# Kernel tuning notes

Hardware: AMD Instinct MI355X
Metric: run time of the kernel (lower is better)

## Reference

```python
import jax, jax.numpy as jnp
import numpy as np

EMB = 768
HEADS = 12
HEAD_DIM = EMB // HEADS
SEQ = 4096
BATCH = 1


def setup_inputs() -> dict:
    key = jax.random.key(0)
    ks = jax.random.split(key, 9)
    s = 1.0 / np.sqrt(EMB)
    return {
        "x": jax.random.normal(ks[0], (BATCH, SEQ, EMB), dtype=jnp.float32),
        "wq": jax.random.normal(ks[1], (EMB, EMB), dtype=jnp.float32) * s,
        "bq": jax.random.normal(ks[2], (EMB,), dtype=jnp.float32) * s,
        "wk": jax.random.normal(ks[3], (EMB, EMB), dtype=jnp.float32) * s,
        "bk": jax.random.normal(ks[4], (EMB,), dtype=jnp.float32) * s,
        "wv": jax.random.normal(ks[5], (EMB, EMB), dtype=jnp.float32) * s,
        "bv": jax.random.normal(ks[6], (EMB,), dtype=jnp.float32) * s,
        "wo": jax.random.normal(ks[7], (EMB, EMB), dtype=jnp.float32) * s,
        "bo": jax.random.normal(ks[8], (EMB,), dtype=jnp.float32) * s,
    }


def reference(x, wq, bq, wk, bk, wv, bv, wo, bo):
    b, n, _ = x.shape
    # projections: [b, n, emb] -> [b, heads, n, head_dim]
    def split_heads(t):
        return t.reshape(b, n, HEADS, HEAD_DIM).transpose(0, 2, 1, 3)
    q = split_heads(x @ wq + bq)
    k = split_heads(x @ wk + bk)
    v = split_heads(x @ wv + bv)
    # full N x N scores (naive attention, as in the original)
    scores = jnp.einsum("bhqd,bhkd->bhqk", q, k)
    causal = jnp.triu(jnp.ones((n, n), dtype=bool), k=1)
    scores = jnp.where(causal, -jnp.inf, scores)
    weights = jax.nn.softmax(scores / np.sqrt(HEAD_DIM), axis=-1)
    # dropout with rate 0.0 is identity (eval mode)
    ctx = jnp.einsum("bhqk,bhkd->bhqd", weights, v)
    ctx = ctx.transpose(0, 2, 1, 3).reshape(b, n, EMB)
    return ctx @ wo + bo
```

## Files before the change

### kernel.cpp

```cpp
#include <hip/hip_runtime.h>
#include <stdint.h>

#define SEQ 4096
#define EMB 768
#define HEADS 12
#define HD 64
#define NQT (SEQ / 64)

typedef __attribute__((ext_vector_type(8))) short short8;
typedef __attribute__((ext_vector_type(4))) short short4v;
typedef __attribute__((ext_vector_type(8))) __bf16 bf16x8;
typedef __attribute__((ext_vector_type(4))) __bf16 bf16x4;
typedef __attribute__((ext_vector_type(4))) float f32x4;

#define QSCALE 0.18033688011112043f

static __device__ __forceinline__ unsigned short f2bf(float f) {
    unsigned int u = __builtin_bit_cast(unsigned int, f);
    unsigned int r = 0x7fffu + ((u >> 16) & 1u);
    u += r;
    return (unsigned short)(u >> 16);
}

static __device__ __forceinline__ f32x4 mfma32(short8 a, short8 b, f32x4 c) {
    return __builtin_amdgcn_mfma_f32_16x16x32_bf16(
        __builtin_bit_cast(bf16x8, a), __builtin_bit_cast(bf16x8, b), c, 0, 0, 0);
}

static __device__ __forceinline__ f32x4 mfma16(short4v a, short4v b, f32x4 c) {
#if __has_builtin(__builtin_amdgcn_mfma_f32_16x16x16_bf16)
    return __builtin_amdgcn_mfma_f32_16x16x16_bf16(
        __builtin_bit_cast(bf16x4, a), __builtin_bit_cast(bf16x4, b), c, 0, 0, 0);
#else
    return __builtin_amdgcn_mfma_f32_16x16x16bf16_1k(a, b, c, 0, 0, 0);
#endif
}

static __device__ __forceinline__ short4v pack4bf(float a, float b, float c, float d) {
#if __has_builtin(__builtin_amdgcn_cvt_pk_bf16_f32)
    typedef __attribute__((ext_vector_type(2))) __bf16 bf16x2;
    bf16x2 lo = __builtin_amdgcn_cvt_pk_bf16_f32(a, b);
    bf16x2 hi = __builtin_amdgcn_cvt_pk_bf16_f32(c, d);
    uint2 u = {__builtin_bit_cast(unsigned int, lo), __builtin_bit_cast(unsigned int, hi)};
    return __builtin_bit_cast(short4v, u);
#else
    short4v p;
    p[0] = (short)f2bf(a); p[1] = (short)f2bf(b);
    p[2] = (short)f2bf(c); p[3] = (short)f2bf(d);
    return p;
#endif
}

static __device__ __forceinline__ void load_lds16(const void* g, void* l) {
    __builtin_amdgcn_global_load_lds(
        (const __attribute__((address_space(1))) unsigned int*)(uintptr_t)g,
        (__attribute__((address_space(3))) unsigned int*)(uintptr_t)l, 16, 0, 0);
}

__global__ __launch_bounds__(256) void convert_x(const float* __restrict__ x,
                                                 unsigned short* __restrict__ xb) {
    int i = blockIdx.x * 256 + threadIdx.x;
    float4 v = ((const float4*)x)[i];
    ushort4 o = {f2bf(v.x), f2bf(v.y), f2bf(v.z), f2bf(v.w)};
    ((ushort4*)xb)[i] = o;
}

__global__ __launch_bounds__(256) void convert_w(const float* __restrict__ wq,
                                                 const float* __restrict__ wk,
                                                 const float* __restrict__ wv,
                                                 const float* __restrict__ wo,
                                                 unsigned short* __restrict__ wqkvT,
                                                 unsigned short* __restrict__ woT) {
    __shared__ float Ls[64][65];
    const int z = blockIdx.z;
    const float* W = (z == 0) ? wq : (z == 1) ? wk : (z == 2) ? wv : wo;
    unsigned short* dst = (z < 3) ? (wqkvT + (size_t)z * EMB * EMB) : woT;
    const int k0 = blockIdx.x * 64, n0 = blockIdx.y * 64;
    const int r = threadIdx.x >> 2, c0 = (threadIdx.x & 3) * 16;
    for (int j = 0; j < 16; j += 4) {
        float4 v = *(const float4*)&W[(size_t)(k0 + r) * EMB + n0 + c0 + j];
        Ls[r][c0 + j] = v.x;
        Ls[r][c0 + j + 1] = v.y;
        Ls[r][c0 + j + 2] = v.z;
        Ls[r][c0 + j + 3] = v.w;
    }
    __syncthreads();
    unsigned short tmp[16];
    for (int j = 0; j < 16; j++) tmp[j] = f2bf(Ls[c0 + j][r]);
    *(uint4*)&dst[(size_t)(n0 + r) * EMB + k0 + c0] = *(uint4*)tmp;
    *(uint4*)&dst[(size_t)(n0 + r) * EMB + k0 + c0 + 8] = *(uint4*)(tmp + 8);
}

template <int MODE>
__global__ __launch_bounds__(256) void gemm128(const unsigned short* __restrict__ A,
                                               const unsigned short* __restrict__ Bt,
                                               const float* __restrict__ b0p,
                                               const float* __restrict__ b1p,
                                               const float* __restrict__ b2p,
                                               unsigned short* __restrict__ QKb,
                                               unsigned short* __restrict__ Vtb,
                                               float* __restrict__ outp) {
    __shared__ __align__(16) unsigned short As[128 * 32];
    __shared__ __align__(16) unsigned short Bs[128 * 32];
    const int tid = threadIdx.x;
    const int wave = tid >> 6, lane = tid & 63, quad = lane >> 4, l16 = lane & 15;
    const int m0 = blockIdx.x * 128, n0 = blockIdx.y * 128;
    const int wm = (wave >> 1) * 64, wn = (wave & 1) * 64;
    const int lrow = lane >> 2, lcol = (lane & 3) * 8;

    f32x4 acc[4][4] = {};

    for (int k0 = 0; k0 < EMB; k0 += 32) {
        __syncthreads();
        for (int t = 0; t < 2; t++) {
            int row = wave * 32 + t * 16 + lrow;
            load_lds16(&A[(size_t)(m0 + row) * EMB + k0 + lcol], &As[(wave * 2 + t) * 512]);
            load_lds16(&Bt[(size_t)(n0 + row) * EMB + k0 + lcol], &Bs[(wave * 2 + t) * 512]);
        }
        __syncthreads();
        short8 a[4], b[4];
        for (int i = 0; i < 4; i++) a[i] = *(const short8*)&As[(wm + i * 16 + l16) * 32 + quad * 8];
        for (int i = 0; i < 4; i++) b[i] = *(const short8*)&Bs[(wn + i * 16 + l16) * 32 + quad * 8];
        for (int i = 0; i < 4; i++)
            for (int j = 0; j < 4; j++) acc[i][j] = mfma32(a[i], b[j], acc[i][j]);
    }

    if (MODE == 1) {
        for (int i = 0; i < 4; i++)
            for (int j = 0; j < 4; j++) {
                int mbase = m0 + wm + i * 16 + quad * 4;
                int n = n0 + wn + j * 16 + l16;
                float bv = b0p[n];
                for (int r = 0; r < 4; r++) outp[(size_t)(mbase + r) * EMB + n] = acc[i][j][r] + bv;
            }
    } else {
        const int z = n0 / EMB;
        if (z < 2) {
            const float* bias = z ? b1p : b0p;
            const float sc = z ? 1.0f : QSCALE;
            for (int i = 0; i < 4; i++)
                for (int j = 0; j < 4; j++) {
                    int mbase = m0 + wm + i * 16 + quad * 4;
                    int n = n0 + wn + j * 16 + l16;
                    float bv = bias[n - z * EMB];
                    for (int r = 0; r < 4; r++)
                        QKb[(size_t)(mbase + r) * 1536 + n] = f2bf((acc[i][j][r] + bv) * sc);
                }
        } else {
            for (int i = 0; i < 4; i++)
                for (int j = 0; j < 4; j++) {
                    int mbase = m0 + wm + i * 16 + quad * 4;
                    int nn = n0 + wn + j * 16 + l16 - 2 * EMB;
                    int h = nn >> 6, d = nn & 63;
                    float bv = b2p[nn];
                    ushort4 pk;
                    pk.x = f2bf(acc[i][j][0] + bv);
                    pk.y = f2bf(acc[i][j][1] + bv);
                    pk.z = f2bf(acc[i][j][2] + bv);
                    pk.w = f2bf(acc[i][j][3] + bv);
                    *(ushort4*)&Vtb[(size_t)(h * HD + d) * SEQ + mbase] = pk;
                }
        }
    }
}

__global__ __launch_bounds__(256) void attn_kernel(const unsigned short* __restrict__ QKb,
                                                   const unsigned short* __restrict__ Vtb,
                                                   unsigned short* __restrict__ ctxb,
                                                   unsigned short* __restrict__ Op,
                                                   float* __restrict__ mArr,
                                                   float* __restrict__ lArr) {
    __shared__ __align__(16) unsigned short Qs[64 * 72];
    __shared__ __align__(16) unsigned short Ks[64 * 72];
    __shared__ __align__(16) unsigned short Vs[64 * 72];

    const int bid = blockIdx.x;
    int s, h, qt, kb, ke;
    if (bid < 768) {
        s = bid & 1;
        int idx = bid >> 1;
        qt = 63 - idx / 12;
        h = idx % 12;
        int h0 = (qt + 2) >> 1;
        kb = s ? h0 : 0;
        ke = s ? qt : h0 - 1;
    } else {
        s = -1;
        int idx = bid - 768;
        qt = 31 - idx / 12;
        h = idx % 12;
        kb = 0;
        ke = qt;
    }
    const int qbase = qt * 64;
    const int tid = threadIdx.x;
    const int wave = tid >> 6, lane = tid & 63, quad = lane >> 4, l16 = lane & 15;

    const unsigned short* Qg = QKb + (size_t)h * HD;
    const unsigned short* Kg = QKb + (size_t)(EMB + h * HD);
    const unsigned short* Vh = Vtb + (size_t)h * HD * SEQ;

    const int row = tid >> 2, cg = (tid & 3) * 16;
    *(uint4*)&Qs[row * 72 + cg] = *(const uint4*)&Qg[(size_t)(qbase + row) * 1536 + cg];
    *(uint4*)&Qs[row * 72 + cg + 8] = *(const uint4*)&Qg[(size_t)(qbase + row) * 1536 + cg + 8];
    __syncthreads();
    const short8 bQ0 = *(const short8*)&Qs[(wave * 16 + l16) * 72 + quad * 8];
    const short8 bQ1 = *(const short8*)&Qs[(wave * 16 + l16) * 72 + 32 + quad * 8];
    const int q = qbase + wave * 16 + l16;

    f32x4 O[4] = {};
    float m_i = -3.0e38f, l_i = 0.f;

    uint4 kr0, kr1, vr0, vr1;
    {
        const int kb64 = kb * 64;
        kr0 = *(const uint4*)&Kg[(size_t)(kb64 + row) * 1536 + cg];
        kr1 = *(const uint4*)&Kg[(size_t)(kb64 + row) * 1536 + cg + 8];
        vr0 = *(const uint4*)&Vh[(size_t)row * SEQ + kb64 + cg];
        vr1 = *(const uint4*)&Vh[(size_t)row * SEQ + kb64 + cg + 8];
    }

    for (int kt = kb; kt <= ke; kt++) {
        const int kbase = kt * 64;
        __syncthreads();
        *(uint4*)&Ks[row * 72 + cg] = kr0;
        *(uint4*)&Ks[row * 72 + cg + 8] = kr1;
        *(uint4*)&Vs[row * 72 + cg] = vr0;
        *(uint4*)&Vs[row * 72 + cg + 8] = vr1;
        if (kt < ke) {
            const int nb = kbase + 64;
            kr0 = *(const uint4*)&Kg[(size_t)(nb + row) * 1536 + cg];
            kr1 = *(const uint4*)&Kg[(size_t)(nb + row) * 1536 + cg + 8];
            vr0 = *(const uint4*)&Vh[(size_t)row * SEQ + nb + cg];
            vr1 = *(const uint4*)&Vh[(size_t)row * SEQ + nb + cg + 8];
        }
        __syncthreads();

        f32x4 st[4];
        for (int nt = 0; nt < 4; nt++) {
            short8 aK0 = *(const short8*)&Ks[(nt * 16 + l16) * 72 + quad * 8];
            short8 aK1 = *(const short8*)&Ks[(nt * 16 + l16) * 72 + 32 + quad * 8];
            f32x4 z = {};
            z = mfma32(aK0, bQ0, z);
            z = mfma32(aK1, bQ1, z);
            st[nt] = z;
        }
        if (kt == qt) {
            for (int nt = 0; nt < 4; nt++)
                for (int r = 0; r < 4; r++)
                    if (kbase + nt * 16 + quad * 4 + r > q) st[nt][r] = -INFINITY;
        }
        float mx = -3.0e38f;
        for (int nt = 0; nt < 4; nt++)
            for (int r = 0; r < 4; r++) mx = fmaxf(mx, st[nt][r]);
        mx = fmaxf(mx, __shfl_xor(mx, 16));
        mx = fmaxf(mx, __shfl_xor(mx, 32));
        const bool inc = mx > m_i;
        if (__ballot(inc)) {
            const float mn = inc ? mx : m_i;
            const float alpha = __builtin_amdgcn_exp2f(m_i - mn);
            m_i = mn;
            l_i *= alpha;
            for (int dt = 0; dt < 4; dt++)
                for (int r = 0; r < 4; r++) O[dt][r] *= alpha;
        }
        float rs = 0.f;
        short4v pk[4];
        for (int nt = 0; nt < 4; nt++) {
            float p0 = __builtin_amdgcn_exp2f(st[nt][0] - m_i);
            float p1 = __builtin_amdgcn_exp2f(st[nt][1] - m_i);
            float p2 = __builtin_amdgcn_exp2f(st[nt][2] - m_i);
            float p3 = __builtin_amdgcn_exp2f(st[nt][3] - m_i);
            rs += p0 + p1 + p2 + p3;
            pk[nt] = pack4bf(p0, p1, p2, p3);
        }
        rs += __shfl_xor(rs, 16);
        rs += __shfl_xor(rs, 32);
        l_i += rs;
        for (int dt = 0; dt < 4; dt++)
            for (int nt = 0; nt < 4; nt++) {
                short4v av = *(const short4v*)&Vs[(dt * 16 + l16) * 72 + nt * 16 + quad * 4];
                O[dt] = mfma16(av, pk[nt], O[dt]);
            }
    }

    const int ql = wave * 16 + l16;
    if (s < 0) {
        const float inv = 1.f / l_i;
        for (int dt = 0; dt < 4; dt++) {
            ushort4 o;
            o.x = f2bf(O[dt][0] * inv);
            o.y = f2bf(O[dt][1] * inv);
            o.z = f2bf(O[dt][2] * inv);
            o.w = f2bf(O[dt][3] * inv);
            *(ushort4*)&ctxb[(size_t)q * EMB + h * HD + dt * 16 + quad * 4] = o;
        }
    } else {
        const int pb = (s * HEADS + h) * 32 + (qt - 32);
        for (int dt = 0; dt < 4; dt++) {
            ushort4 o;
            o.x = f2bf(O[dt][0]);
            o.y = f2bf(O[dt][1]);
            o.z = f2bf(O[dt][2]);
            o.w = f2bf(O[dt][3]);
            *(ushort4*)&Op[(size_t)pb * 4096 + ql * 64 + dt * 16 + quad * 4] = o;
        }
        if (quad == 0) {
            mArr[pb * 64 + ql] = m_i;
            lArr[pb * 64 + ql] = l_i;
        }
    }
}

__global__ __launch_bounds__(256) void merge_kernel(const unsigned short* __restrict__ Op,
                                                    const float* __restrict__ mArr,
                                                    const float* __restrict__ lArr,
                                                    unsigned short* __restrict__ ctxb) {
    const int idx = blockIdx.x;
    const int qt = 32 + idx / HEADS;
    const int h = idx % HEADS;
    const int q = threadIdx.x >> 2, d0 = (threadIdx.x & 3) * 16;
    const int pb0 = h * 32 + (qt - 32);
    const int pb1 = (HEADS + h) * 32 + (qt - 32);
    const float m0 = mArr[pb0 * 64 + q], m1 = mArr[pb1 * 64 + q];
    const float l0 = lArr[pb0 * 64 + q], l1 = lArr[pb1 * 64 + q];
    const float M = fmaxf(m0, m1);
    float a0 = __builtin_amdgcn_exp2f(m0 - M);
    float a1 = __builtin_amdgcn_exp2f(m1 - M);
    const float inv = 1.f / (a0 * l0 + a1 * l1);
    a0 *= inv;
    a1 *= inv;
    for (int jj = 0; jj < 16; jj += 8) {
        uint4 u0 = *(const uint4*)&Op[(size_t)pb0 * 4096 + q * 64 + d0 + jj];
        uint4 u1 = *(const uint4*)&Op[(size_t)pb1 * 4096 + q * 64 + d0 + jj];
        const unsigned short* p0 = (const unsigned short*)&u0;
        const unsigned short* p1 = (const unsigned short*)&u1;
        unsigned short o[8];
        for (int t = 0; t < 8; t++) {
            float f0 = __builtin_bit_cast(float, (unsigned int)p0[t] << 16);
            float f1 = __builtin_bit_cast(float, (unsigned int)p1[t] << 16);
            o[t] = f2bf(a0 * f0 + a1 * f1);
        }
        *(uint4*)&ctxb[(size_t)(qt * 64 + q) * EMB + h * HD + d0 + jj] = *(uint4*)o;
    }
}

extern "C" void kernel_launch(void* const* d_in, const int* in_sizes, int n_in,
                              void* d_out, int out_size, void* d_ws, size_t ws_size,
                              hipStream_t stream) {
    const float* x = (const float*)d_in[0];
    const float* wq = (const float*)d_in[1];
    const float* bq = (const float*)d_in[2];
    const float* wk = (const float*)d_in[3];
    const float* bk = (const float*)d_in[4];
    const float* wv = (const float*)d_in[5];
    const float* bv = (const float*)d_in[6];
    const float* wo = (const float*)d_in[7];
    const float* bo = (const float*)d_in[8];

    unsigned short* ws = (unsigned short*)d_ws;
    unsigned short* xb = ws;
    unsigned short* wqkvT = xb + SEQ * EMB;
    unsigned short* woT = wqkvT + 3 * EMB * EMB;
    unsigned short* QKb = woT + EMB * EMB;
    unsigned short* Vtb = QKb + (size_t)SEQ * 1536;
    unsigned short* ctxb = Vtb + HEADS * SEQ * HD;
    unsigned short* Op = xb;
    float* mArr = (float*)wqkvT;
    float* lArr = mArr + 768 * 64;

    convert_x<<<dim3(SEQ * EMB / 4 / 256), 256, 0, stream>>>(x, xb);
    convert_w<<<dim3(12, 12, 4), 256, 0, stream>>>(wq, wk, wv, wo, wqkvT, woT);
    gemm128<0><<<dim3(SEQ / 128, 3 * EMB / 128), 256, 0, stream>>>(
        xb, wqkvT, bq, bk, bv, QKb, Vtb, nullptr);
    attn_kernel<<<dim3(1152), 256, 0, stream>>>(QKb, Vtb, ctxb, Op, mArr, lArr);
    merge_kernel<<<dim3(384), 256, 0, stream>>>(Op, mArr, lArr, ctxb);
    gemm128<1><<<dim3(SEQ / 128, EMB / 128), 256, 0, stream>>>(
        ctxb, woT, bo, nullptr, nullptr, nullptr, nullptr, (float*)d_out);
}
```

Before: 209.2 us.

## Rebalance causal attention split, swizzle LDS, fuse converts, shrink output GEMM tile

Merges the two conversion kernels into one launch. Causal attention now splits query tiles into 1, 2 or 3 key-range chunks by depth, which evens out block work across 1440 blocks. Chunk 0 writes straight into ctx, and merge combines up to three partials. Q fragments are loaded directly from global memory. K/V LDS use XOR swizzles in place of padding. The output projection uses 64x128 tiles to launch more blocks. Risks include extra partial traffic, the correctness of the merge-buffer aliasing, and more complex indexing.

After: 209.5 us. No clear change (+0.1%).

```diff
diff --git a/kernel.cpp b/kernel.cpp
--- a/kernel.cpp
+++ b/kernel.cpp
@@ -57,25 +57,29 @@
         (__attribute__((address_space(3))) unsigned int*)(uintptr_t)l, 16, 0, 0);
 }
 
-__global__ __launch_bounds__(256) void convert_x(const float* __restrict__ x,
-                                                 unsigned short* __restrict__ xb) {
-    int i = blockIdx.x * 256 + threadIdx.x;
-    float4 v = ((const float4*)x)[i];
-    ushort4 o = {f2bf(v.x), f2bf(v.y), f2bf(v.z), f2bf(v.w)};
-    ((ushort4*)xb)[i] = o;
-}
-
-__global__ __launch_bounds__(256) void convert_w(const float* __restrict__ wq,
-                                                 const float* __restrict__ wk,
-                                                 const float* __restrict__ wv,
-                                                 const float* __restrict__ wo,
-                                                 unsigned short* __restrict__ wqkvT,
-                                                 unsigned short* __restrict__ woT) {
+__global__ __launch_bounds__(256) void convert_all(const float* __restrict__ x,
+                                                   const float* __restrict__ wq,
+                                                   const float* __restrict__ wk,
+                                                   const float* __restrict__ wv,
+                                                   const float* __restrict__ wo,
+                                                   unsigned short* __restrict__ xb,
+                                                   unsigned short* __restrict__ wqkvT,
+                                                   unsigned short* __restrict__ woT) {
     __shared__ float Ls[64][65];
-    const int z = blockIdx.z;
+    const int bid = blockIdx.x;
+    if (bid < 3072) {
+        int i = bid * 256 + threadIdx.x;
+        float4 v = ((const float4*)x)[i];
+        ushort4 o = {f2bf(v.x), f2bf(v.y), f2bf(v.z), f2bf(v.w)};
+        ((ushort4*)xb)[i] = o;
+        return;
+    }
+    const int idx = bid - 3072;
+    const int z = idx / 144;
+    const int bx = (idx % 144) / 12, by = idx % 12;
     const float* W = (z == 0) ? wq : (z == 1) ? wk : (z == 2) ? wv : wo;
     unsigned short* dst = (z < 3) ? (wqkvT + (size_t)z * EMB * EMB) : woT;
-    const int k0 = blockIdx.x * 64, n0 = blockIdx.y * 64;
+    const int k0 = bx * 64, n0 = by * 64;
     const int r = threadIdx.x >> 2, c0 = (threadIdx.x & 3) * 16;
     for (int j = 0; j < 16; j += 4) {
         float4 v = *(const float4*)&W[(size_t)(k0 + r) * EMB + n0 + c0 + j];
@@ -91,15 +95,13 @@
     *(uint4*)&dst[(size_t)(n0 + r) * EMB + k0 + c0 + 8] = *(uint4*)(tmp + 8);
 }
 
-template <int MODE>
-__global__ __launch_bounds__(256) void gemm128(const unsigned short* __restrict__ A,
-                                               const unsigned short* __restrict__ Bt,
-                                               const float* __restrict__ b0p,
-                                               const float* __restrict__ b1p,
-                                               const float* __restrict__ b2p,
-                                               unsigned short* __restrict__ QKb,
-                                               unsigned short* __restrict__ Vtb,
-                                               float* __restrict__ outp) {
+__global__ __launch_bounds__(256) void gemm_qkv(const unsigned short* __restrict__ A,
+                                                const unsigned short* __restrict__ Bt,
+                                                const float* __restrict__ b0p,
+                                                const float* __restrict__ b1p,
+                                                const float* __restrict__ b2p,
+                                                unsigned short* __restrict__ QKb,
+                                                unsigned short* __restrict__ Vtb) {
     __shared__ __align__(16) unsigned short As[128 * 32];
     __shared__ __align__(16) unsigned short Bs[128 * 32];
     const int tid = threadIdx.x;
@@ -125,43 +127,71 @@
             for (int j = 0; j < 4; j++) acc[i][j] = mfma32(a[i], b[j], acc[i][j]);
     }
 
-    if (MODE == 1) {
+    const int z = n0 / EMB;
+    if (z < 2) {
+        const float* bias = z ? b1p : b0p;
+        const float sc = z ? 1.0f : QSCALE;
         for (int i = 0; i < 4; i++)
             for (int j = 0; j < 4; j++) {
                 int mbase = m0 + wm + i * 16 + quad * 4;
                 int n = n0 + wn + j * 16 + l16;
-                float bv = b0p[n];
-                for (int r = 0; r < 4; r++) outp[(size_t)(mbase + r) * EMB + n] = acc[i][j][r] + bv;
+                float bv = bias[n - z * EMB];
+                for (int r = 0; r < 4; r++)
+                    QKb[(size_t)(mbase + r) * 1536 + n] = f2bf((acc[i][j][r] + bv) * sc);
             }
     } else {
-        const int z = n0 / EMB;
-        if (z < 2) {
-            const float* bias = z ? b1p : b0p;
-            const float sc = z ? 1.0f : QSCALE;
-            for (int i = 0; i < 4; i++)
-                for (int j = 0; j < 4; j++) {
-                    int mbase = m0 + wm + i * 16 + quad * 4;
-                    int n = n0 + wn + j * 16 + l16;
-                    float bv = bias[n - z * EMB];
-                    for (int r = 0; r < 4; r++)
-                        QKb[(size_t)(mbase + r) * 1536 + n] = f2bf((acc[i][j][r] + bv) * sc);
-                }
-        } else {
-            for (int i = 0; i < 4; i++)
-                for (int j = 0; j < 4; j++) {
-                    int mbase = m0 + wm + i * 16 + quad * 4;
-                    int nn = n0 + wn + j * 16 + l16 - 2 * EMB;
-                    int h = nn >> 6, d = nn & 63;
-                    float bv = b2p[nn];
-                    ushort4 pk;
-                    pk.x = f2bf(acc[i][j][0] + bv);
-                    pk.y = f2bf(acc[i][j][1] + bv);
-                    pk.z = f2bf(acc[i][j][2] + bv);
-                    pk.w = f2bf(acc[i][j][3] + bv);
-                    *(ushort4*)&Vtb[(size_t)(h * HD + d) * SEQ + mbase] = pk;
-                }
-        }
-    }
+        for (int i = 0; i < 4; i++)
+            for (int j = 0; j < 4; j++) {
+                int mbase = m0 + wm + i * 16 + quad * 4;
+                int nn = n0 + wn + j * 16 + l16 - 2 * EMB;
+                int h = nn >> 6, d = nn & 63;
+                float bv = b2p[nn];
+                ushort4 pk;
+                pk.x = f2bf(acc[i][j][0] + bv);
+                pk.y = f2bf(acc[i][j][1] + bv);
+                pk.z = f2bf(acc[i][j][2] + bv);
+                pk.w = f2bf(acc[i][j][3] + bv);
+                *(ushort4*)&Vtb[(size_t)(h * HD + d) * SEQ + mbase] = pk;
+            }
+    }
+}
+
+__global__ __launch_bounds__(256) void gemm_out(const unsigned short* __restrict__ A,
+                                                const unsigned short* __restrict__ Bt,
+                                                const float* __restrict__ bias,
+                                                float* __restrict__ outp) {
+    __shared__ __align__(16) unsigned short As[64 * 32];
+    __shared__ __align__(16) unsigned short Bs[128 * 32];
+    const int tid = threadIdx.x;
+    const int wave = tid >> 6, lane = tid & 63, quad = lane >> 4, l16 = lane & 15;
+    const int m0 = blockIdx.x * 64, n0 = blockIdx.y * 128;
+    const int wm = (wave >> 1) * 32, wn = (wave & 1) * 64;
+    const int lrow = lane >> 2, lcol = (lane & 3) * 8;
+
+    f32x4 acc[2][4] = {};
+
+    for (int k0 = 0; k0 < EMB; k0 += 32) {
+        __syncthreads();
+        load_lds16(&A[(size_t)(m0 + wave * 16 + lrow) * EMB + k0 + lcol], &As[wave * 512]);
+        for (int t = 0; t < 2; t++) {
+            int row = wave * 32 + t * 16 + lrow;
+            load_lds16(&Bt[(size_t)(n0 + row) * EMB + k0 + lcol], &Bs[(wave * 2 + t) * 512]);
+        }
+        __syncthreads();
+        short8 a[2], b[4];
+        for (int i = 0; i < 2; i++) a[i] = *(const short8*)&As[(wm + i * 16 + l16) * 32 + quad * 8];
+        for (int j = 0; j < 4; j++) b[j] = *(const short8*)&Bs[(wn + j * 16 + l16) * 32 + quad * 8];
+        for (int i = 0; i < 2; i++)
+            for (int j = 0; j < 4; j++) acc[i][j] = mfma32(a[i], b[j], acc[i][j]);
+    }
+
+    for (int i = 0; i < 2; i++)
+        for (int j = 0; j < 4; j++) {
+            int mbase = m0 + wm + i * 16 + quad * 4;
+            int n = n0 + wn + j * 16 + l16;
+            float bv = bias[n];
+            for (int r = 0; r < 4; r++) outp[(size_t)(mbase + r) * EMB + n] = acc[i][j][r] + bv;
+        }
 }
 
 __global__ __launch_bounds__(256) void attn_kernel(const unsigned short* __restrict__ QKb,
@@ -170,28 +200,24 @@
                                                    unsigned short* __restrict__ Op,
                                                    float* __restrict__ mArr,
                                                    float* __restrict__ lArr) {
-    __shared__ __align__(16) unsigned short Qs[64 * 72];
-    __shared__ __align__(16) unsigned short Ks[64 * 72];
-    __shared__ __align__(16) unsigned short Vs[64 * 72];
+    __shared__ __align__(16) unsigned short Ks[64 * 64];
+    __shared__ __align__(16) unsigned short Vs[64 * 64];
 
     const int bid = blockIdx.x;
-    int s, h, qt, kb, ke;
-    if (bid < 768) {
-        s = bid & 1;
-        int idx = bid >> 1;
-        qt = 63 - idx / 12;
-        h = idx % 12;
-        int h0 = (qt + 2) >> 1;
-        kb = s ? h0 : 0;
-        ke = s ? qt : h0 - 1;
+    const int h = bid / 120;
+    const int rem = bid % 120;
+    int qt, ch, nch;
+    if (rem < 24) {
+        qt = rem; ch = 0; nch = 1;
+    } else if (rem < 72) {
+        int q2 = rem - 24;
+        qt = 24 + (q2 >> 1); ch = q2 & 1; nch = 2;
     } else {
-        s = -1;
-        int idx = bid - 768;
-        qt = 31 - idx / 12;
-        h = idx % 12;
-        kb = 0;
-        ke = qt;
-    }
+        int q3 = rem - 72;
+        qt = 48 + q3 / 3; ch = q3 % 3; nch = 3;
+    }
+    const int kb = (ch * (qt + 1)) / nch;
+    const int ke = ((ch + 1) * (qt + 1)) / nch - 1;
     const int qbase = qt * 64;
     const int tid = threadIdx.x;
     const int wave = tid >> 6, lane = tid & 63, quad = lane >> 4, l16 = lane & 15;
@@ -200,13 +226,12 @@
     const unsigned short* Kg = QKb + (size_t)(EMB + h * HD);
     const unsigned short* Vh = Vtb + (size_t)h * HD * SEQ;
 
-    const int row = tid >> 2, cg = (tid & 3) * 16;
-    *(uint4*)&Qs[row * 72 + cg] = *(const uint4*)&Qg[(size_t)(qbase + row) * 1536 + cg];
-    *(uint4*)&Qs[row * 72 + cg + 8] = *(const uint4*)&Qg[(size_t)(qbase + row) * 1536 + cg + 8];
-    __syncthreads();
-    const short8 bQ0 = *(const short8*)&Qs[(wave * 16 + l16) * 72 + quad * 8];
-    const short8 bQ1 = *(const short8*)&Qs[(wave * 16 + l16) * 72 + 32 + quad * 8];
     const int q = qbase + wave * 16 + l16;
+    const short8 bQ0 = *(const short8*)&Qg[(size_t)q * 1536 + quad * 8];
+    const short8 bQ1 = *(const short8*)&Qg[(size_t)q * 1536 + 32 + quad * 8];
+
+    const int row = tid >> 2, t4 = tid & 3, cg = t4 * 16;
+    const int swk = row & 7, swv = row & 15;
 
     f32x4 O[4] = {};
     float m_i = -3.0e38f, l_i = 0.f;
@@ -223,10 +248,12 @@
     for (int kt = kb; kt <= ke; kt++) {
         const int kbase = kt * 64;
         __syncthreads();
-        *(uint4*)&Ks[row * 72 + cg] = kr0;
-        *(uint4*)&Ks[row * 72 + cg + 8] = kr1;
-        *(uint4*)&Vs[row * 72 + cg] = vr0;
-        *(uint4*)&Vs[row * 72 + cg + 8] = vr1;
+        *(uint4*)&Ks[row * 64 + ((2 * t4) ^ swk) * 8] = kr0;
+        *(uint4*)&Ks[row * 64 + ((2 * t4 + 1) ^ swk) * 8] = kr1;
+        *(uint2*)&Vs[row * 64 + ((4 * t4) ^ swv) * 4] = ((const uint2*)&vr0)[0];
+        *(uint2*)&Vs[row * 64 + ((4 * t4 + 1) ^ swv) * 4] = ((const uint2*)&vr0)[1];
+        *(uint2*)&Vs[row * 64 + ((4 * t4 + 2) ^ swv) * 4] = ((const uint2*)&vr1)[0];
+        *(uint2*)&Vs[row * 64 + ((4 * t4 + 3) ^ swv) * 4] = ((const uint2*)&vr1)[1];
         if (kt < ke) {
             const int nb = kbase + 64;
             kr0 = *(const uint4*)&Kg[(size_t)(nb + row) * 1536 + cg];
@@ -236,10 +263,11 @@
         }
         __syncthreads();
 
+        const int swr = l16 & 7;
         f32x4 st[4];
         for (int nt = 0; nt < 4; nt++) {
-            short8 aK0 = *(const short8*)&Ks[(nt * 16 + l16) * 72 + quad * 8];
-            short8 aK1 = *(const short8*)&Ks[(nt * 16 + l16) * 72 + 32 + quad * 8];
+            short8 aK0 = *(const short8*)&Ks[(nt * 16 + l16) * 64 + (quad ^ swr) * 8];
+            short8 aK1 = *(const short8*)&Ks[(nt * 16 + l16) * 64 + ((quad + 4) ^ swr) * 8];
             f32x4 z = {};
             z = mfma32(aK0, bQ0, z);
             z = mfma32(aK1, bQ1, z);
@@ -279,13 +307,13 @@
         l_i += rs;
         for (int dt = 0; dt < 4; dt++)
             for (int nt = 0; nt < 4; nt++) {
-                short4v av = *(const short4v*)&Vs[(dt * 16 + l16) * 72 + nt * 16 + quad * 4];
+                short4v av = *(const short4v*)&Vs[(dt * 16 + l16) * 64 + ((4 * nt + quad) ^ l16) * 4];
                 O[dt] = mfma16(av, pk[nt], O[dt]);
             }
     }
 
     const int ql = wave * 16 + l16;
-    if (s < 0) {
+    if (nch == 1) {
         const float inv = 1.f / l_i;
         for (int dt = 0; dt < 4; dt++) {
             ushort4 o;
@@ -296,18 +324,31 @@
             *(ushort4*)&ctxb[(size_t)q * EMB + h * HD + dt * 16 + quad * 4] = o;
         }
     } else {
-        const int pb = (s * HEADS + h) * 32 + (qt - 32);
-        for (int dt = 0; dt < 4; dt++) {
-            ushort4 o;
-            o.x = f2bf(O[dt][0]);
-            o.y = f2bf(O[dt][1]);
-            o.z = f2bf(O[dt][2]);
-            o.w = f2bf(O[dt][3]);
-            *(ushort4*)&Op[(size_t)pb * 4096 + ql * 64 + dt * 16 + quad * 4] = o;
+        if (ch == 0) {
+            for (int dt = 0; dt < 4; dt++) {
+                ushort4 o;
+                o.x = f2bf(O[dt][0]);
+                o.y = f2bf(O[dt][1]);
+                o.z = f2bf(O[dt][2]);
+                o.w = f2bf(O[dt][3]);
+                *(ushort4*)&ctxb[(size_t)q * EMB + h * HD + dt * 16 + quad * 4] = o;
+            }
+        } else {
+            const int pid = (qt < 48) ? h * 56 + (qt - 24)
+                                      : h * 56 + 24 + (qt - 48) * 2 + (ch - 1);
+            for (int dt = 0; dt < 4; dt++) {
+                ushort4 o;
+                o.x = f2bf(O[dt][0]);
+                o.y = f2bf(O[dt][1]);
+                o.z = f2bf(O[dt][2]);
+                o.w = f2bf(O[dt][3]);
+                *(ushort4*)&Op[(size_t)pid * 4096 + ql * 64 + dt * 16 + quad * 4] = o;
+            }
         }
         if (quad == 0) {
-            mArr[pb * 64 + ql] = m_i;
-            lArr[pb * 64 + ql] = l_i;
+            const int mli = ((h * 64 + qt) * 3 + ch) * 64 + ql;
+            mArr[mli] = m_i;
+            lArr[mli] = l_i;
         }
     }
 }
@@ -316,32 +357,46 @@
                                                     const float* __restrict__ mArr,
                                                     const float* __restrict__ lArr,
                                                     unsigned short* __restrict__ ctxb) {
-    const int idx = blockIdx.x;
-    const int qt = 32 + idx / HEADS;
-    const int h = idx % HEADS;
+    const int gid = blockIdx.x;
+    const int h = gid / 40;
+    const int qt = 24 + gid % 40;
+    const int nch = qt / 24 + 1;
     const int q = threadIdx.x >> 2, d0 = (threadIdx.x & 3) * 16;
-    const int pb0 = h * 32 + (qt - 32);
-    const int pb1 = (HEADS + h) * 32 + (qt - 32);
-    const float m0 = mArr[pb0 * 64 + q], m1 = mArr[pb1 * 64 + q];
-    const float l0 = lArr[pb0 * 64 + q], l1 = lArr[pb1 * 64 + q];
-    const float M = fmaxf(m0, m1);
-    float a0 = __builtin_amdgcn_exp2f(m0 - M);
-    float a1 = __builtin_amdgcn_exp2f(m1 - M);
-    const float inv = 1.f / (a0 * l0 + a1 * l1);
-    a0 *= inv;
-    a1 *= inv;
+    const int mlbase = (h * 64 + qt) * 3;
+
+    float mc[3], lc[3];
+    for (int c = 0; c < nch; c++) {
+        mc[c] = mArr[(mlbase + c) * 64 + q];
+        lc[c] = lArr[(mlbase + c) * 64 + q];
+    }
+    float M = mc[0];
+    for (int c = 1; c < nch; c++) M = fmaxf(M, mc[c]);
+    float w[3], L = 0.f;
+    for (int c = 0; c < nch; c++) {
+        w[c] = __builtin_amdgcn_exp2f(mc[c] - M);
+        L += w[c] * lc[c];
+    }
+    const float inv = 1.f / L;
+    for (int c = 0; c < nch; c++) w[c] *= inv;
+
+    unsigned short* dst = &ctxb[(size_t)(qt * 64 + q) * EMB + h * HD + d0];
     for (int jj = 0; jj < 16; jj += 8) {
-        uint4 u0 = *(const uint4*)&Op[(size_t)pb0 * 4096 + q * 64 + d0 + jj];
-        uint4 u1 = *(const uint4*)&Op[(size_t)pb1 * 4096 + q * 64 + d0 + jj];
+        uint4 u0 = *(const uint4*)&dst[jj];
+        float f[8];
         const unsigned short* p0 = (const unsigned short*)&u0;
-        const unsigned short* p1 = (const unsigned short*)&u1;
+        for (int t = 0; t < 8; t++)
+            f[t] = w[0] * __builtin_bit_cast(float, (unsigned int)p0[t] << 16);
+        for (int c = 1; c < nch; c++) {
+            const int pid = (qt < 48) ? h * 56 + (qt - 24)
+                                      : h * 56 + 24 + (qt - 48) * 2 + (c - 1);
+            uint4 u = *(const uint4*)&Op[(size_t)pid * 4096 + q * 64 + d0 + jj];
+            const unsigned short* p = (const unsigned short*)&u;
+            for (int t = 0; t < 8; t++)
+                f[t] += w[c] * __builtin_bit_cast(float, (unsigned int)p[t] << 16);
+        }
         unsigned short o[8];
-        for (int t = 0; t < 8; t++) {
-            float f0 = __builtin_bit_cast(float, (unsigned int)p0[t] << 16);
-            float f1 = __builtin_bit_cast(float, (unsigned int)p1[t] << 16);
-            o[t] = f2bf(a0 * f0 + a1 * f1);
-        }
-        *(uint4*)&ctxb[(size_t)(qt * 64 + q) * EMB + h * HD + d0 + jj] = *(uint4*)o;
+        for (int t = 0; t < 8; t++) o[t] = f2bf(f[t]);
+        *(uint4*)&dst[jj] = *(uint4*)o;
     }
 }
 
@@ -367,14 +422,12 @@
     unsigned short* ctxb = Vtb + HEADS * SEQ * HD;
     unsigned short* Op = xb;
     float* mArr = (float*)wqkvT;
-    float* lArr = mArr + 768 * 64;
-
-    convert_x<<<dim3(SEQ * EMB / 4 / 256), 256, 0, stream>>>(x, xb);
-    convert_w<<<dim3(12, 12, 4), 256, 0, stream>>>(wq, wk, wv, wo, wqkvT, woT);
-    gemm128<0><<<dim3(SEQ / 128, 3 * EMB / 128), 256, 0, stream>>>(
-        xb, wqkvT, bq, bk, bv, QKb, Vtb, nullptr);
-    attn_kernel<<<dim3(1152), 256, 0, stream>>>(QKb, Vtb, ctxb, Op, mArr, lArr);
-    merge_kernel<<<dim3(384), 256, 0, stream>>>(Op, mArr, lArr, ctxb);
-    gemm128<1><<<dim3(SEQ / 128, EMB / 128), 256, 0, stream>>>(
-        ctxb, woT, bo, nullptr, nullptr, nullptr, nullptr, (float*)d_out);
-}
+    float* lArr = mArr + 2304 * 64;
+
+    convert_all<<<dim3(3072 + 576), 256, 0, stream>>>(x, wq, wk, wv, wo, xb, wqkvT, woT);
+    gemm_qkv<<<dim3(SEQ / 128, 3 * EMB / 128), 256, 0, stream>>>(
+        xb, wqkvT, bq, bk, bv, QKb, Vtb);
+    attn_kernel<<<dim3(1440), 256, 0, stream>>>(QKb, Vtb, ctxb, Op, mArr, lArr);
+    merge_kernel<<<dim3(480), 256, 0, stream>>>(Op, mArr, lArr, ctxb);
+    gemm_out<<<dim3(SEQ / 64, EMB / 128), 256, 0, stream>>>(ctxb, woT, bo, (float*)d_out);
+}
```
